# Kernel optimization log

Measured on AMD Instinct MI355X. Metric: run time of the kernel, lower is better.

The kernel has to match this reference:

```python
import jax, jax.numpy as jnp
import numpy as np

N_NODES = 50000
N_EDGES = 800000
IN_C, HID_C, OUT_C = 128, 128, 1


def setup_inputs() -> dict:
    key = jax.random.key(0)
    ks = jax.random.split(key, 10)
    x = jax.random.normal(ks[0], (N_NODES, IN_C), dtype=jnp.float32)
    x2 = jax.random.normal(ks[1], (1,), dtype=jnp.float32)
    edge_index = jax.random.randint(ks[2], (2, N_EDGES), 0, N_NODES, dtype=jnp.int64)
    # GCNConv params (glorot-ish scale) and final linear
    W1 = jax.random.normal(ks[3], (IN_C, HID_C), dtype=jnp.float32) / np.sqrt(IN_C)
    b1 = jnp.zeros((HID_C,), dtype=jnp.float32)
    W2 = jax.random.normal(ks[4], (HID_C, HID_C), dtype=jnp.float32) / np.sqrt(HID_C)
    b2 = jnp.zeros((HID_C,), dtype=jnp.float32)
    Wlin = jax.random.normal(ks[5], (HID_C, OUT_C), dtype=jnp.float32) / np.sqrt(HID_C)
    blin = jnp.zeros((OUT_C,), dtype=jnp.float32)
    return {"x": x, "x2": x2, "edge_index": edge_index, "num_nodes": N_NODES,
            "W1": W1, "b1": b1, "W2": W2, "b2": b2, "Wlin": Wlin, "blin": blin}


def _gcn_conv(h, W, b, src, dst, norm, num_nodes):
    # linear transform then normalized scatter-add aggregation (PyG GCNConv)
    h = h @ W  # [N, C_out]
    msg = h[src] * norm[:, None]  # gather + scale, [E+N, C_out]
    out = jax.ops.segment_sum(msg, dst, num_segments=num_nodes)
    return out + b


def _gcn_norm(edge_index, num_nodes):
    # add self-loops, compute sym-normalization coefficients D^-1/2 A D^-1/2
    loop = jnp.arange(num_nodes, dtype=edge_index.dtype)
    src = jnp.concatenate([edge_index[0], loop])
    dst = jnp.concatenate([edge_index[1], loop])
    ones = jnp.ones(src.shape[0], dtype=jnp.float32)
    deg = jax.ops.segment_sum(ones, dst, num_segments=num_nodes)
    dinv = jnp.where(deg > 0, jax.lax.rsqrt(deg), 0.0)
    norm = dinv[src] * dinv[dst]
    return src, dst, norm


def reference(x, x2, edge_index, num_nodes, W1, b1, W2, b2, Wlin, blin):
    src, dst, norm = _gcn_norm(edge_index, num_nodes)
    h = _gcn_conv(x, W1, b1, src, dst, norm, num_nodes)
    h = jax.nn.relu(h)
    # dropout is identity in eval mode
    h = _gcn_conv(h, W2, b2, src, dst, norm, num_nodes)
    h = jax.nn.relu(h)
    out = h @ Wlin + blin  # [N, 1]
    return out.squeeze(-1)
```

## Files before the change

kernel.cpp:

```cpp
#include <hip/hip_runtime.h>
#include <hip/hip_bf16.h>

#define N_NODES 50000
#define N_EDGES 800000
#define C 128

#define NBB   391
#define CAPB  3072
#define CAPC  3456
#define CHUNK 2048

#define NSL     4
#define SL_U4   200000
#define SL_US   1600000
#define BPS     3125

typedef __attribute__((ext_vector_type(8))) short short8v;
typedef __attribute__((ext_vector_type(4))) float f32x4;

__device__ __forceinline__ unsigned int bf16rtn(float f) {
    unsigned int u = __float_as_uint(f);
    return (u + 0x7fffu + ((u >> 16) & 1u)) >> 16;
}
__device__ __forceinline__ unsigned int packbf2(float lo, float hi) {
    return bf16rtn(lo) | (bf16rtn(hi) << 16);
}

__global__ void k_prepW(const float* __restrict__ W1, const float* __restrict__ W2,
                        unsigned short* __restrict__ Wsplit, int* __restrict__ gcur) {
    int t = blockIdx.x * 256 + threadIdx.x;
    if (t < NBB) gcur[t] = 0;
    if (t >= 32768) return;
    int layer = t >> 14, idx = t & 16383;
    int i = idx >> 7, j = idx & 127;
    const float* Wsrc = layer ? W2 : W1;
    float w = Wsrc[i * 128 + j];
    unsigned int h = bf16rtn(w);
    float hf = __uint_as_float(h << 16);
    unsigned int l = bf16rtn(w - hf);
    unsigned short* base = Wsplit + layer * 32768;
    base[j * 128 + i] = (unsigned short)h;
    base[16384 + j * 128 + i] = (unsigned short)l;
}

__global__ __launch_bounds__(256) void k_binA(const int* __restrict__ ei,
                                              int* __restrict__ gcur,
                                              int2* __restrict__ tmp) {
    __shared__ int hist[NBB];
    __shared__ int lbase[NBB];
    __shared__ int gbaseL[NBB];
    __shared__ int wsum[4];
    __shared__ int2 buf[CHUNK];
    __shared__ int totalv;

    int tid = threadIdx.x;
    int e0 = blockIdx.x * CHUNK;

    for (int i = tid; i < NBB; i += 256) hist[i] = 0;
    __syncthreads();

    int sarr[8], darr[8], parr[8];
#pragma unroll
    for (int j = 0; j < 8; ++j) {
        int e = e0 + j * 256 + tid;
        darr[j] = -1;
        if (e < N_EDGES) {
            sarr[j] = ei[e];
            int d = ei[N_EDGES + e];
            darr[j] = d;
            parr[j] = atomicAdd(&hist[d >> 7], 1);
        }
    }
    __syncthreads();

    {
        int i0 = 2 * tid, i1 = i0 + 1;
        int c0 = (i0 < NBB) ? hist[i0] : 0;
        int c1 = (i1 < NBB) ? hist[i1] : 0;
        int c = c0 + c1;
        int lane = tid & 63, w = tid >> 6;
        int s = c;
#pragma unroll
        for (int d = 1; d < 64; d <<= 1) {
            int u = __shfl_up(s, d, 64);
            if (lane >= d) s += u;
        }
        if (lane == 63) wsum[w] = s;
        __syncthreads();
        int add = 0;
        for (int i = 0; i < w; ++i) add += wsum[i];
        int incl = s + add;
        int excl = incl - c;
        if (i0 < NBB) lbase[i0] = excl;
        if (i1 < NBB) lbase[i1] = excl + c0;
        if (tid == 255) totalv = incl;
    }
    for (int i = tid; i < NBB; i += 256) {
        int cnt = hist[i];
        int run = (cnt > 0) ? atomicAdd(&gcur[i], cnt) : 0;
        gbaseL[i] = i * CAPB + run;
    }
    __syncthreads();

#pragma unroll
    for (int j = 0; j < 8; ++j) {
        if (darr[j] >= 0) {
            int b = darr[j] >> 7;
            buf[lbase[b] + parr[j]] = make_int2(sarr[j], darr[j]);
        }
    }
    __syncthreads();

    int total = totalv;
    for (int i = tid; i < total; i += 256) {
        int2 v = buf[i];
        int b = v.y >> 7;
        int gpos = gbaseL[b] + (i - lbase[b]);
        if (gpos < (b + 1) * CAPB) tmp[gpos] = v;
    }
}

__global__ __launch_bounds__(256) void k_csr(const int2* __restrict__ tmp,
                                             const int* __restrict__ gcur,
                                             int* __restrict__ csr,
                                             int* __restrict__ offn,
                                             int* __restrict__ degn,
                                             float* __restrict__ dinv) {
    __shared__ int   rawsrc[CAPB];
    __shared__ short rawloc[CAPB];
    __shared__ int   lcnt[128];
    __shared__ int   lbase[128];
    __shared__ int   lcur[128];

    int b = blockIdx.x, tid = threadIdx.x;
    int cnt = gcur[b];
    if (cnt > CAPB) cnt = CAPB;

    if (tid < 128) { lcnt[tid] = 0; lcur[tid] = 0; }
    __syncthreads();

    const int2* tmpb = tmp + (size_t)b * CAPB;
    for (int i = tid; i < cnt; i += 256) {
        int2 v = tmpb[i];
        int l = v.y & 127;
        rawsrc[i] = v.x;
        rawloc[i] = (short)l;
        atomicAdd(&lcnt[l], 1);
    }
    __syncthreads();

    if (tid < 64) {
        int c0 = lcnt[2 * tid], c1 = lcnt[2 * tid + 1];
        int p0 = (c0 + 3) & ~3, p1 = (c1 + 3) & ~3;
        int c = p0 + p1;
        int s = c;
#pragma unroll
        for (int d = 1; d < 64; d <<= 1) {
            int u = __shfl_up(s, d, 64);
            if (tid >= d) s += u;
        }
        int excl = s - c;
        lbase[2 * tid] = excl;
        lbase[2 * tid + 1] = excl + p0;
    }
    __syncthreads();

    int node = b * 128 + tid;
    if (tid < 128 && node < N_NODES) {
        offn[node] = b * CAPC + lbase[tid];
        degn[node] = lcnt[tid];
        dinv[node] = rsqrtf((float)lcnt[tid] + 1.0f);
    }

    for (int i = tid; i < cnt; i += 256) {
        int l = rawloc[i];
        int p = atomicAdd(&lcur[l], 1);
        csr[b * CAPC + lbase[l] + p] = rawsrc[i];
    }
}

template <bool AF32>
__global__ __launch_bounds__(512, 4) void k_gemm(const void* __restrict__ Ain,
                                                 const unsigned short* __restrict__ Whg,
                                                 const unsigned short* __restrict__ Wlg,
                                                 const float* __restrict__ dinv,
                                                 unsigned short* __restrict__ Hout) {
    __shared__ uint4 Al[64 * 16];
    __shared__ float ddv[64];

    int tid = threadIdx.x;
    int row0 = blockIdx.x * 64;
    int wv = tid >> 6, lane = tid & 63;
    int col = wv * 16 + (lane & 15);
    int kq = lane >> 4;

    const uint4* Bh4 = (const uint4*)Whg;
    const uint4* Bl4 = (const uint4*)Wlg;
    short8v bh[4], bl[4];
#pragma unroll
    for (int ks = 0; ks < 4; ++ks) {
        uint4 uh = Bh4[col * 16 + ks * 4 + kq];
        uint4 ul = Bl4[col * 16 + ks * 4 + kq];
        bh[ks] = *reinterpret_cast<short8v*>(&uh);
        bl[ks] = *reinterpret_cast<short8v*>(&ul);
    }

#pragma unroll
    for (int pass = 0; pass < 2; ++pass) {
        int row = (tid >> 4) + pass * 32;
        int o = tid & 15;
        int gr = row0 + row;
        uint4 u = make_uint4(0u, 0u, 0u, 0u);
        if (AF32) {
            float4 v0 = make_float4(0.f, 0.f, 0.f, 0.f), v1 = v0;
            if (gr < N_NODES) {
                const float4* A4 = (const float4*)Ain;
                v0 = A4[gr * 32 + o * 2];
                v1 = A4[gr * 32 + o * 2 + 1];
            }
            u.x = packbf2(v0.x, v0.y);
            u.y = packbf2(v0.z, v0.w);
            u.z = packbf2(v1.x, v1.y);
            u.w = packbf2(v1.z, v1.w);
        } else {
            if (gr < N_NODES)
                u = ((const uint4*)Ain)[(size_t)(o >> 2) * SL_U4 + gr * 4 + (o & 3)];
        }
        int byte = (row * 256 + o * 16) ^ ((row & 7) << 4);
        Al[byte >> 4] = u;
    }
    if (tid < 64) {
        int gr = row0 + tid;
        ddv[tid] = (gr < N_NODES) ? dinv[gr] : 0.f;
    }
    __syncthreads();

    f32x4 acc[4];
#pragma unroll
    for (int st = 0; st < 4; ++st) acc[st] = (f32x4){0.f, 0.f, 0.f, 0.f};

#pragma unroll
    for (int st = 0; st < 4; ++st) {
        int rowl = st * 16 + (lane & 15);
        int rbase = rowl * 256;
        int swz = (rowl & 7) << 4;
#pragma unroll
        for (int ks = 0; ks < 4; ++ks) {
            int byte = (rbase + ks * 64 + kq * 16) ^ swz;
            uint4 ua = Al[byte >> 4];
            short8v a = *reinterpret_cast<short8v*>(&ua);
            acc[st] = __builtin_amdgcn_mfma_f32_16x16x32_bf16(a, bh[ks], acc[st], 0, 0, 0);
            acc[st] = __builtin_amdgcn_mfma_f32_16x16x32_bf16(a, bl[ks], acc[st], 0, 0, 0);
        }
    }

    {
        int sl = col >> 5, cs = col & 31;
        unsigned short* Hs = Hout + (size_t)sl * SL_US + cs;
#pragma unroll
        for (int st = 0; st < 4; ++st) {
#pragma unroll
            for (int r = 0; r < 4; ++r) {
                int rowl = st * 16 + kq * 4 + r;
                int gr = row0 + rowl;
                if (gr < N_NODES)
                    Hs[gr * 32] = (unsigned short)bf16rtn(ddv[rowl] * acc[st][r]);
            }
        }
    }
}

__device__ __forceinline__ void add8(float* acc, uint4 u) {
    acc[0] += __uint_as_float(u.x << 16);
    acc[1] += __uint_as_float(u.x & 0xffff0000u);
    acc[2] += __uint_as_float(u.y << 16);
    acc[3] += __uint_as_float(u.y & 0xffff0000u);
    acc[4] += __uint_as_float(u.z << 16);
    acc[5] += __uint_as_float(u.z & 0xffff0000u);
    acc[6] += __uint_as_float(u.w << 16);
    acc[7] += __uint_as_float(u.w & 0xffff0000u);
}

template <bool FINAL>
__global__ __launch_bounds__(256) void k_agg(const uint4* __restrict__ hall,
                                             const int* __restrict__ csr,
                                             const int* __restrict__ offn,
                                             const int* __restrict__ degn,
                                             const float* __restrict__ bias,
                                             const float* __restrict__ Wlin,
                                             void* __restrict__ outbuf) {
    int bid = blockIdx.x;
    int slice = bid / BPS;
    int nb = bid - slice * BPS;
    int wv = threadIdx.x >> 6, lane = threadIdx.x & 63;
    int j = lane >> 4;
    int sub = (lane >> 2) & 3;
    int cq = lane & 3;
    int n = nb * 16 + wv * 4 + j;

    const uint4* hs = hall + (size_t)slice * SL_U4;

    int o0 = offn[n];
    int deg = degn[n];
    uint4 us = hs[n * 4 + cq];

    float acc[8];
#pragma unroll
    for (int k = 0; k < 8; ++k) acc[k] = 0.f;

    int e = o0 + sub;
    int end = o0 + deg;
    for (; e < end; e += 4) {
        int s = __builtin_nontemporal_load(csr + e);
        uint4 u = hs[s * 4 + cq];
        add8(acc, u);
    }
#pragma unroll
    for (int k = 0; k < 8; ++k) {
        acc[k] += __shfl_xor(acc[k], 4, 64);
        acc[k] += __shfl_xor(acc[k], 8, 64);
    }

    float dv = rsqrtf((float)deg + 1.0f);
    float hv[8];
    hv[0] = __uint_as_float(us.x << 16); hv[1] = __uint_as_float(us.x & 0xffff0000u);
    hv[2] = __uint_as_float(us.y << 16); hv[3] = __uint_as_float(us.y & 0xffff0000u);
    hv[4] = __uint_as_float(us.z << 16); hv[5] = __uint_as_float(us.z & 0xffff0000u);
    hv[6] = __uint_as_float(us.w << 16); hv[7] = __uint_as_float(us.w & 0xffff0000u);
    float4 bv0 = ((const float4*)bias)[slice * 8 + cq * 2];
    float4 bv1 = ((const float4*)bias)[slice * 8 + cq * 2 + 1];
    float o[8];
    o[0] = dv * (acc[0] + hv[0]) + bv0.x;
    o[1] = dv * (acc[1] + hv[1]) + bv0.y;
    o[2] = dv * (acc[2] + hv[2]) + bv0.z;
    o[3] = dv * (acc[3] + hv[3]) + bv0.w;
    o[4] = dv * (acc[4] + hv[4]) + bv1.x;
    o[5] = dv * (acc[5] + hv[5]) + bv1.y;
    o[6] = dv * (acc[6] + hv[6]) + bv1.z;
    o[7] = dv * (acc[7] + hv[7]) + bv1.w;

    if (!FINAL) {
        if (sub == 0) {
            uint4 u;
            u.x = packbf2(fmaxf(o[0], 0.f), fmaxf(o[1], 0.f));
            u.y = packbf2(fmaxf(o[2], 0.f), fmaxf(o[3], 0.f));
            u.z = packbf2(fmaxf(o[4], 0.f), fmaxf(o[5], 0.f));
            u.w = packbf2(fmaxf(o[6], 0.f), fmaxf(o[7], 0.f));
            ((uint4*)outbuf)[(size_t)slice * SL_U4 + n * 4 + cq] = u;
        }
    } else {
        float4 wl0 = ((const float4*)Wlin)[slice * 8 + cq * 2];
        float4 wl1 = ((const float4*)Wlin)[slice * 8 + cq * 2 + 1];
        float v = fmaxf(o[0], 0.f) * wl0.x + fmaxf(o[1], 0.f) * wl0.y
                + fmaxf(o[2], 0.f) * wl0.z + fmaxf(o[3], 0.f) * wl0.w
                + fmaxf(o[4], 0.f) * wl1.x + fmaxf(o[5], 0.f) * wl1.y
                + fmaxf(o[6], 0.f) * wl1.z + fmaxf(o[7], 0.f) * wl1.w;
        v += __shfl_xor(v, 1, 64);
        v += __shfl_xor(v, 2, 64);
        if ((lane & 15) == 0)
            __builtin_nontemporal_store(v, (float*)outbuf + slice * N_NODES + n);
    }
}

__global__ void k_fin(const float* __restrict__ partial, const float* __restrict__ blin,
                      float* __restrict__ out) {
    int n = blockIdx.x * 256 + threadIdx.x;
    if (n < N_NODES)
        out[n] = ((partial[n] + partial[N_NODES + n])
                + (partial[2 * N_NODES + n] + partial[3 * N_NODES + n])) + blin[0];
}

extern "C" void kernel_launch(void* const* d_in, const int* in_sizes, int n_in,
                              void* d_out, int out_size, void* d_ws, size_t ws_size,
                              hipStream_t stream) {
    const float* x    = (const float*)d_in[0];
    const int*   ei   = (const int*)d_in[2];
    const float* W1   = (const float*)d_in[4];
    const float* b1   = (const float*)d_in[5];
    const float* W2   = (const float*)d_in[6];
    const float* b2   = (const float*)d_in[7];
    const float* Wlin = (const float*)d_in[8];
    const float* blin = (const float*)d_in[9];
    float* out = (float*)d_out;

    char* ws = (char*)d_ws;
    size_t off = 0;
    auto carve = [&](size_t bytes) -> void* {
        void* p = ws + off;
        off = (off + bytes + 255) & ~(size_t)255;
        return p;
    };
    int*   gcur = (int*)  carve(NBB * sizeof(int));
    float* dinv = (float*)carve(N_NODES * sizeof(float));
    int*   offn = (int*)  carve(N_NODES * sizeof(int));
    int*   degn = (int*)  carve(N_NODES * sizeof(int));
    int2*  tmp  = (int2*) carve((size_t)NBB * CAPB * sizeof(int2));
    int*   csr  = (int*)  carve((size_t)NBB * CAPC * sizeof(int));
    unsigned short* hbf  = (unsigned short*)carve((size_t)NSL * SL_US * sizeof(unsigned short));
    unsigned short* hbf2 = (unsigned short*)carve((size_t)NSL * SL_US * sizeof(unsigned short));
    float* partial = (float*)carve((size_t)NSL * N_NODES * sizeof(float));
    unsigned short* wsplit = (unsigned short*)carve(4 * 16384 * sizeof(unsigned short));

    const int NB_A = (N_EDGES + CHUNK - 1) / CHUNK;
    const int NB_G = (N_NODES + 63) / 64;
    const int NB_S = NSL * BPS;
    const int NB_F = (N_NODES + 255) / 256;

    const unsigned short* W1h = wsplit;
    const unsigned short* W1l = wsplit + 16384;
    const unsigned short* W2h = wsplit + 32768;
    const unsigned short* W2l = wsplit + 49152;

    k_prepW<<<128, 256, 0, stream>>>(W1, W2, wsplit, gcur);
    k_binA<<<NB_A, 256, 0, stream>>>(ei, gcur, tmp);
    k_csr<<<NBB, 256, 0, stream>>>(tmp, gcur, csr, offn, degn, dinv);

    k_gemm<true><<<NB_G, 512, 0, stream>>>(x, W1h, W1l, dinv, hbf);
    k_agg<false><<<NB_S, 256, 0, stream>>>((const uint4*)hbf, csr, offn, degn,
                                           b1, Wlin, hbf2);
    k_gemm<false><<<NB_G, 512, 0, stream>>>(hbf2, W2h, W2l, dinv, hbf);
    k_agg<true><<<NB_S, 256, 0, stream>>>((const uint4*)hbf, csr, offn, degn,
                                          b2, Wlin, partial);
    k_fin<<<NB_F, 256, 0, stream>>>(partial, blin, out);
}
```

Before: 238.1 us.

## Assign one wavefront per node in aggregation with 16-way edge parallelism

Remaps the aggregation kernel so each wavefront processes a single node, with 16 lane groups splitting its edges instead of 4 lanes per node over 4 nodes. The main loop reads two CSR indices per lane as int2 and falls back to 16-edge and remainder steps. This quadruples the block count and adds two shuffle-reduction stages. It is meant to cut per-lane serial edge iterations and raise memory-level parallelism, at the cost of idle lanes on low-degree nodes.

```diff
diff --git a/kernel.cpp b/kernel.cpp
--- a/kernel.cpp
+++ b/kernel.cpp
@@ -13,7 +13,7 @@
 #define NSL     4
 #define SL_U4   200000
 #define SL_US   1600000
-#define BPS     3125
+#define BPS     12500
 
 typedef __attribute__((ext_vector_type(8))) short short8v;
 typedef __attribute__((ext_vector_type(4))) float f32x4;
@@ -293,32 +293,49 @@
     int slice = bid / BPS;
     int nb = bid - slice * BPS;
     int wv = threadIdx.x >> 6, lane = threadIdx.x & 63;
-    int j = lane >> 4;
-    int sub = (lane >> 2) & 3;
+    int eg = lane >> 2;
     int cq = lane & 3;
-    int n = nb * 16 + wv * 4 + j;
+    int n = nb * 4 + wv;
 
     const uint4* hs = hall + (size_t)slice * SL_U4;
 
     int o0 = offn[n];
     int deg = degn[n];
+    int end = o0 + deg;
+
     uint4 us = hs[n * 4 + cq];
 
     float acc[8];
 #pragma unroll
     for (int k = 0; k < 8; ++k) acc[k] = 0.f;
 
-    int e = o0 + sub;
-    int end = o0 + deg;
-    for (; e < end; e += 4) {
-        int s = __builtin_nontemporal_load(csr + e);
+    int e = o0;
+    for (; e + 32 <= end; e += 32) {
+        int2 s2 = *(const int2*)(csr + e + 2 * eg);
+        uint4 u0 = hs[s2.x * 4 + cq];
+        uint4 u1 = hs[s2.y * 4 + cq];
+        add8(acc, u0);
+        add8(acc, u1);
+    }
+    if (e + 16 <= end) {
+        int s = __builtin_nontemporal_load(csr + e + eg);
         uint4 u = hs[s * 4 + cq];
         add8(acc, u);
+        e += 16;
+    }
+    {
+        int rem = end - e;
+        if (eg < rem) {
+            int s = __builtin_nontemporal_load(csr + e + eg);
+            add8(acc, hs[s * 4 + cq]);
+        }
     }
 #pragma unroll
     for (int k = 0; k < 8; ++k) {
         acc[k] += __shfl_xor(acc[k], 4, 64);
         acc[k] += __shfl_xor(acc[k], 8, 64);
+        acc[k] += __shfl_xor(acc[k], 16, 64);
+        acc[k] += __shfl_xor(acc[k], 32, 64);
     }
 
     float dv = rsqrtf((float)deg + 1.0f);
@@ -340,7 +357,7 @@
     o[7] = dv * (acc[7] + hv[7]) + bv1.w;
 
     if (!FINAL) {
-        if (sub == 0) {
+        if (eg == 0) {
             uint4 u;
             u.x = packbf2(fmaxf(o[0], 0.f), fmaxf(o[1], 0.f));
             u.y = packbf2(fmaxf(o[2], 0.f), fmaxf(o[3], 0.f));
@@ -357,7 +374,7 @@
                 + fmaxf(o[6], 0.f) * wl1.z + fmaxf(o[7], 0.f) * wl1.w;
         v += __shfl_xor(v, 1, 64);
         v += __shfl_xor(v, 2, 64);
-        if ((lane & 15) == 0)
+        if ((lane & 3) == 0 && eg == 0)
             __builtin_nontemporal_store(v, (float*)outbuf + slice * N_NODES + n);
     }
 }
```

Result: slower. 299.1 us (+25.7%).
